# Optimization experiments

Measured on AMD Instinct MI355X. Metric: run time of the kernel, lower is better.

The kernel has to match this reference:

```python
import jax, jax.numpy as jnp
import numpy as np

NUM_HEADS = 16


def setup_inputs() -> dict:
    key = jax.random.key(0)
    ks = jax.random.split(key, 9)
    B, S, C = 2, 2048, 1024
    s = 1.0 / np.sqrt(C)
    return {
        "hidden_states": jax.random.normal(ks[0], (B, S, C), jnp.float32),
        "Wq": jax.random.normal(ks[1], (C, C), jnp.float32) * s,
        "bq": jnp.zeros((C,), jnp.float32),
        "Wk": jax.random.normal(ks[2], (C, C), jnp.float32) * s,
        "bk": jnp.zeros((C,), jnp.float32),
        "Wv": jax.random.normal(ks[3], (C, C), jnp.float32) * s,
        "bv": jnp.zeros((C,), jnp.float32),
        "Wo": jax.random.normal(ks[4], (C, C), jnp.float32) * s,
        "bo": jnp.zeros((C,), jnp.float32),
    }


def reference(hidden_states, Wq, bq, Wk, bk, Wv, bv, Wo, bo):
    # Self-attention path of AttnProcessor (3D input, no mask, no norms,
    # residual_connection=True, rescale_output_factor=1.0).
    B, S, C = hidden_states.shape
    H = NUM_HEADS
    D = C // H
    residual = hidden_states

    q = hidden_states @ Wq + bq  # [B,S,C]
    k = hidden_states @ Wk + bk
    v = hidden_states @ Wv + bv

    # head_to_batch_dim: [B,S,C] -> [B,S,H,D]
    q = q.reshape(B, S, H, D)
    k = k.reshape(B, S, H, D)
    v = v.reshape(B, S, H, D)

    scale = 1.0 / np.sqrt(D).astype(np.float32)
    # get_attention_scores: baddbmm with scale, then softmax (full [B,H,S,S])
    scores = jnp.einsum("bqhd,bkhd->bhqk", q, k) * scale
    probs = jax.nn.softmax(scores, axis=-1)

    out = jnp.einsum("bhqk,bkhd->bqhd", probs, v)  # bmm(probs, value)
    out = out.reshape(B, S, C)  # batch_to_head_dim

    out = out @ Wo + bo  # to_out[0]; to_out[1] is dropout (identity in eval)
    out = out + residual  # residual_connection
    return out  # rescale_output_factor = 1.0
```

## Files before the change

### kernel.cpp

```cpp
#include <hip/hip_runtime.h>

#define BATCH 2
#define SEQ   2048
#define CH    1024
#define NHEAD 16
#define HDIM  64
#define MROWS (BATCH * SEQ)

typedef __attribute__((ext_vector_type(8))) short short8;
typedef __attribute__((ext_vector_type(4))) float floatx4;
typedef unsigned short ushort_t;

__device__ __forceinline__ float b2f(ushort_t u) {
    union { unsigned int i; float f; } x;
    x.i = ((unsigned int)u) << 16;
    return x.f;
}
__device__ __forceinline__ ushort_t f2b(float f) {
    union { float f; unsigned int i; } x;
    x.f = f;
    unsigned int lsb = (x.i >> 16) & 1u;
    x.i += 0x7fffu + lsb;
    return (ushort_t)(x.i >> 16);
}
__device__ __forceinline__ unsigned pack2(float a, float b) {
    return (unsigned)f2b(a) | ((unsigned)f2b(b) << 16);
}
__device__ __forceinline__ unsigned cvt_pk_bf16(float a, float b) {
    unsigned r;
    asm("v_cvt_pk_bf16_f32 %0, %1, %2" : "=v"(r) : "v"(a), "v"(b));
    return r;
}

__device__ __forceinline__ void gld16(const ushort_t* g, ushort_t* l) {
    __builtin_amdgcn_global_load_lds(
        (const __attribute__((address_space(1))) void*)g,
        (__attribute__((address_space(3))) void*)l, 16, 0, 0);
}

template <int VM>
__device__ __forceinline__ void vm_barrier() {
    asm volatile("s_waitcnt vmcnt(%0) lgkmcnt(0)\n\ts_barrier" ::"i"(VM)
                 : "memory");
}

__global__ __launch_bounds__(256) void cvt_bf16_kernel(
    const float* __restrict__ in, ushort_t* __restrict__ out, int n4) {
    int i = blockIdx.x * blockDim.x + threadIdx.x;
    if (i < n4) {
        float4 v = ((const float4*)in)[i];
        ushort4 o = {f2b(v.x), f2b(v.y), f2b(v.z), f2b(v.w)};
        ((ushort4*)out)[i] = o;
    }
}

__global__ __launch_bounds__(256) void transpose_cvt_all(
    const float* __restrict__ W0, const float* __restrict__ W1,
    const float* __restrict__ W2, const float* __restrict__ W3,
    ushort_t* __restrict__ T0, ushort_t* __restrict__ T1,
    ushort_t* __restrict__ T2, ushort_t* __restrict__ T3) {
    __shared__ ushort_t T[64][68];
    const int z = blockIdx.z;
    const float* W = (z == 0) ? W0 : (z == 1) ? W1 : (z == 2) ? W2 : W3;
    ushort_t* Wt = (z == 0) ? T0 : (z == 1) ? T1 : (z == 2) ? T2 : T3;
    const int tid = threadIdx.x;
    const int n0 = blockIdx.x * 64, k0 = blockIdx.y * 64;
    const int r = tid >> 4, c4 = (tid & 15) * 4;
#pragma unroll
    for (int p = 0; p < 4; p++) {
        int k = p * 16 + r;
        float4 v = *(const float4*)&W[(size_t)(k0 + k) * CH + n0 + c4];
        T[c4 + 0][k] = f2b(v.x);
        T[c4 + 1][k] = f2b(v.y);
        T[c4 + 2][k] = f2b(v.z);
        T[c4 + 3][k] = f2b(v.w);
    }
    __syncthreads();
#pragma unroll
    for (int p = 0; p < 4; p++) {
        int n = p * 16 + r;
        ushort4 o = {T[n][c4 + 0], T[n][c4 + 1], T[n][c4 + 2], T[n][c4 + 3]};
        *(ushort4*)&Wt[(size_t)(n0 + n) * CH + k0 + c4] = o;
    }
}

__device__ __forceinline__ void gemm_core_db(
    const ushort_t* __restrict__ A, const ushort_t* __restrict__ Bt,
    int bm, int n0, int tid, floatx4 acc[4][4], ushort_t* lds) {
    const int wave = tid >> 6, lane = tid & 63;
    const int quad = lane >> 4, t16 = lane & 15;
    const int wm = wave >> 1, wn = wave & 1;
    const int arow = tid >> 2, ak = (tid & 3) * 8;

    const ushort_t* a0 = A + (size_t)(bm + arow) * CH + ak;
    const ushort_t* a1 = A + (size_t)(bm + 64 + arow) * CH + ak;
    const ushort_t* b0 = Bt + (size_t)(n0 + arow) * CH + ak;
    const ushort_t* b1 = Bt + (size_t)(n0 + 64 + arow) * CH + ak;

#pragma unroll
    for (int i = 0; i < 4; i++)
#pragma unroll
        for (int j = 0; j < 4; j++) acc[i][j] = (floatx4){0.f, 0.f, 0.f, 0.f};

    auto stage = [&](int k, ushort_t* buf) {
        gld16(a0 + k, buf + wave * 512);
        gld16(a1 + k, buf + 2048 + wave * 512);
        gld16(b0 + k, buf + 4096 + wave * 512);
        gld16(b1 + k, buf + 6144 + wave * 512);
    };
    auto compute = [&](const ushort_t* As) {
        const ushort_t* Bs = As + 4096;
        short8 af[4], bf[4];
#pragma unroll
        for (int i = 0; i < 4; i++)
            af[i] = *(const short8*)&As[(wm * 64 + i * 16 + t16) * 32 + quad * 8];
#pragma unroll
        for (int j = 0; j < 4; j++)
            bf[j] = *(const short8*)&Bs[(wn * 64 + j * 16 + t16) * 32 + quad * 8];
#pragma unroll
        for (int i = 0; i < 4; i++)
#pragma unroll
            for (int j = 0; j < 4; j++)
                acc[i][j] = __builtin_amdgcn_mfma_f32_16x16x32_bf16(
                    af[i], bf[j], acc[i][j], 0, 0, 0);
    };

    ushort_t* bcur = lds;
    ushort_t* bnext = lds + 8192;
    ushort_t* bfar = lds + 16384;

    stage(0, bcur);
    stage(32, bnext);

    for (int it = 0; it < CH / 32 - 2; ++it) {
        vm_barrier<4>();
        stage((it + 2) * 32, bfar);
        compute(bcur);
        ushort_t* t = bcur; bcur = bnext; bnext = bfar; bfar = t;
    }
    vm_barrier<4>();
    compute(bcur);
    vm_barrier<0>();
    compute(bnext);
}

__global__ __launch_bounds__(256) void gemm_qkv(
    const ushort_t* __restrict__ X,
    const ushort_t* __restrict__ WqT, const ushort_t* __restrict__ WkT,
    const ushort_t* __restrict__ WvT,
    const float* __restrict__ bq, const float* __restrict__ bk,
    const float* __restrict__ bv,
    ushort_t* __restrict__ Qm, ushort_t* __restrict__ Km,
    ushort_t* __restrict__ Vtm) {
    __shared__ ushort_t lds[3 * 8192];
    const int tid = threadIdx.x;
    const int seg = blockIdx.x >> 3;
    const int n0 = (blockIdx.x & 7) * 128;
    const int bm = blockIdx.y * 128;
    const ushort_t* Bt = (seg == 0) ? WqT : (seg == 1) ? WkT : WvT;
    const float* bias = (seg == 0) ? bq : (seg == 1) ? bk : bv;

    floatx4 acc[4][4];
    gemm_core_db(X, Bt, bm, n0, tid, acc, lds);

    const int lane = tid & 63, wave = tid >> 6;
    const int quad = lane >> 4, t16 = lane & 15;
    const int wm = wave >> 1, wn = wave & 1;

    if (seg < 2) {
        ushort_t* outp = seg ? Km : Qm;
        const float sc = seg ? 1.0f : 0.125f;
#pragma unroll
        for (int i = 0; i < 4; i++)
#pragma unroll
            for (int j = 0; j < 4; j++) {
                const int col = n0 + wn * 64 + j * 16 + t16;
                const float bb = bias[col];
                const int row0 = bm + wm * 64 + i * 16 + quad * 4;
#pragma unroll
                for (int r = 0; r < 4; r++)
                    outp[(size_t)(row0 + r) * CH + col] =
                        f2b((acc[i][j][r] + bb) * sc);
            }
    } else {
        ushort_t* rep = lds;
        const int b = bm >> 11;
        const int s_base = bm & (SEQ - 1);
#pragma unroll
        for (int half = 0; half < 2; half++) {
            __syncthreads();
            if (wn == half) {
#pragma unroll
                for (int i = 0; i < 4; i++)
#pragma unroll
                    for (int j = 0; j < 4; j++) {
                        const int dl = j * 16 + t16;
                        const int sl = wm * 64 + i * 16 + quad * 4;
                        const float bb = bias[n0 + half * 64 + dl];
                        uint2 w = {pack2(acc[i][j][0] + bb, acc[i][j][1] + bb),
                                   pack2(acc[i][j][2] + bb, acc[i][j][3] + bb)};
                        *(uint2*)&rep[dl * 136 + sl] = w;
                    }
            }
            __syncthreads();
#pragma unroll
            for (int step = 0; step < 4; step++) {
                const int dl = step * 16 + (tid >> 4);
                const int sl = (tid & 15) * 8;
                short8 v = *(const short8*)&rep[dl * 136 + sl];
                const int col = n0 + half * 64 + dl;
                const int h = col >> 6, dd = col & 63;
                const int c = (sl >> 3) & 7;
                const int r7 = dd & 7;
                const int slot0 = (c & 4) | ((2 * c) & 3);
                const int slot1 = (c & 4) | ((2 * c + 1) & 3);
                const int sub = ((c >> 1) & 1) << 2;
                ushort_t* vrow = Vtm +
                    (((size_t)b * NHEAD + h) * HDIM + dd) * SEQ + s_base +
                    (sl & 64);
                union { short8 s; uint2 u[2]; } vv;
                vv.s = v;
                *(uint2*)&vrow[((slot0 ^ r7) << 3) + sub] = vv.u[0];
                *(uint2*)&vrow[((slot1 ^ r7) << 3) + sub] = vv.u[1];
            }
        }
    }
}

__global__ __launch_bounds__(256) void gemm_out(
    const ushort_t* __restrict__ Am, const ushort_t* __restrict__ WoT,
    const float* __restrict__ bo, const float* __restrict__ resid,
    float* __restrict__ out) {
    __shared__ ushort_t lds[3 * 6144];
    const int tid = threadIdx.x;
    const int n0 = blockIdx.x * 64;
    const int bm = blockIdx.y * 128;
    const int wave = tid >> 6, lane = tid & 63;
    const int quad = lane >> 4, t16 = lane & 15;
    const int arow = tid >> 2, ak = (tid & 3) * 8;

    const ushort_t* a0 = Am + (size_t)(bm + arow) * CH + ak;
    const ushort_t* a1 = Am + (size_t)(bm + 64 + arow) * CH + ak;
    const ushort_t* b0 = WoT + (size_t)(n0 + arow) * CH + ak;

    floatx4 acc[2][4];
#pragma unroll
    for (int i = 0; i < 2; i++)
#pragma unroll
        for (int j = 0; j < 4; j++) acc[i][j] = (floatx4){0.f, 0.f, 0.f, 0.f};

    auto stage = [&](int k, ushort_t* buf) {
        gld16(a0 + k, buf + wave * 512);
        gld16(a1 + k, buf + 2048 + wave * 512);
        gld16(b0 + k, buf + 4096 + wave * 512);
    };
    auto compute = [&](const ushort_t* As) {
        const ushort_t* Bs = As + 4096;
        short8 af[2], bf[4];
#pragma unroll
        for (int i = 0; i < 2; i++)
            af[i] = *(const short8*)&As[(wave * 32 + i * 16 + t16) * 32 + quad * 8];
#pragma unroll
        for (int j = 0; j < 4; j++)
            bf[j] = *(const short8*)&Bs[(j * 16 + t16) * 32 + quad * 8];
#pragma unroll
        for (int i = 0; i < 2; i++)
#pragma unroll
            for (int j = 0; j < 4; j++)
                acc[i][j] = __builtin_amdgcn_mfma_f32_16x16x32_bf16(
                    af[i], bf[j], acc[i][j], 0, 0, 0);
    };

    ushort_t* bcur = lds;
    ushort_t* bnext = lds + 6144;
    ushort_t* bfar = lds + 12288;

    stage(0, bcur);
    stage(32, bnext);

    for (int it = 0; it < CH / 32 - 2; ++it) {
        vm_barrier<3>();
        stage((it + 2) * 32, bfar);
        compute(bcur);
        ushort_t* t = bcur; bcur = bnext; bnext = bfar; bfar = t;
    }
    vm_barrier<3>();
    compute(bcur);
    vm_barrier<0>();
    compute(bnext);

#pragma unroll
    for (int i = 0; i < 2; i++)
#pragma unroll
        for (int j = 0; j < 4; j++) {
            const int col = n0 + j * 16 + t16;
            const float bb = bo[col];
            const int row0 = bm + wave * 32 + i * 16 + quad * 4;
#pragma unroll
            for (int r = 0; r < 4; r++) {
                const size_t idx = (size_t)(row0 + r) * CH + col;
                out[idx] = acc[i][j][r] + bb + resid[idx];
            }
        }
}

__global__ __launch_bounds__(512, 4) void flash_attn_mfma(
    const ushort_t* __restrict__ Q, const ushort_t* __restrict__ K,
    const ushort_t* __restrict__ Vt, ushort_t* __restrict__ O) {
    __shared__ __attribute__((aligned(16))) ushort_t smem[2][2][64][64];

    const int tid = threadIdx.x;
    const int wave = tid >> 6, lane = tid & 63;
    const int quad = lane >> 4, t16 = lane & 15;
    const int bh = blockIdx.y, b = bh >> 4, h = bh & 15;
    const int q0 = blockIdx.x * 128;

    const size_t base_q = ((size_t)b * SEQ) * CH + (size_t)h * HDIM;
    const size_t base_vt = ((size_t)(b * NHEAD + h)) * HDIM * SEQ;

    short8 qf[2];
    {
        const ushort_t* qp =
            Q + base_q + (size_t)(q0 + wave * 16 + t16) * CH + quad * 8;
        qf[0] = *(const short8*)(qp);
        qf[1] = *(const short8*)(qp + 32);
    }

    const short8 ones = (short8)(short)0x3F80;

    floatx4 Oa[4];
    floatx4 Oe = (floatx4){0.f, 0.f, 0.f, 0.f};
#pragma unroll
    for (int d = 0; d < 4; d++) Oa[d] = (floatx4){0.f, 0.f, 0.f, 0.f};

    const int sr = tid >> 3;
    const int ss = tid & 7;
    const ushort_t* ksrc = K + base_q + (size_t)sr * CH + ((ss ^ (sr & 7)) << 3);
    const ushort_t* vsrc = Vt + base_vt + (size_t)sr * SEQ + (ss << 3);

    auto stage = [&](int k0, int buf) {
        gld16(ksrc + (size_t)k0 * CH, &smem[buf][0][0][0] + wave * 512);
        gld16(vsrc + k0, &smem[buf][1][0][0] + wave * 512);
    };

    const int koff0 = (quad ^ (t16 & 7)) << 3;
    const int koff1 = ((quad + 4) ^ (t16 & 7)) << 3;

    stage(0, 0);

    for (int t = 0; t < SEQ / 64; ++t) {
        vm_barrier<0>();
        if (t + 1 < SEQ / 64) stage((t + 1) * 64, (t + 1) & 1);
        const ushort_t* Kb = &smem[t & 1][0][0][0];
        const ushort_t* Vb = &smem[t & 1][1][0][0];

        uint2 pw[4];
#pragma unroll
        for (int j = 0; j < 4; j++) {
            short8 kf0 = *(const short8*)&Kb[(j * 16 + t16) * 64 + koff0];
            short8 kf1 = *(const short8*)&Kb[(j * 16 + t16) * 64 + koff1];
            floatx4 z = (floatx4){0.f, 0.f, 0.f, 0.f};
            z = __builtin_amdgcn_mfma_f32_16x16x32_bf16(kf0, qf[0], z, 0, 0, 0);
            z = __builtin_amdgcn_mfma_f32_16x16x32_bf16(kf1, qf[1], z, 0, 0, 0);
            pw[j].x = cvt_pk_bf16(__expf(z[0]), __expf(z[1]));
            pw[j].y = cvt_pk_bf16(__expf(z[2]), __expf(z[3]));
        }
        short8 pf0, pf1;
        {
            union { uint4 u; short8 s; } c0, c1;
            c0.u = (uint4){pw[0].x, pw[0].y, pw[1].x, pw[1].y};
            c1.u = (uint4){pw[2].x, pw[2].y, pw[3].x, pw[3].y};
            pf0 = c0.s;
            pf1 = c1.s;
        }

        __builtin_amdgcn_s_setprio(1);
#pragma unroll
        for (int d = 0; d < 4; d++) {
            short8 vf0 = *(const short8*)&Vb[(d * 16 + t16) * 64 + koff0];
            short8 vf1 = *(const short8*)&Vb[(d * 16 + t16) * 64 + koff1];
            Oa[d] = __builtin_amdgcn_mfma_f32_16x16x32_bf16(pf0, vf0, Oa[d], 0, 0, 0);
            Oa[d] = __builtin_amdgcn_mfma_f32_16x16x32_bf16(pf1, vf1, Oa[d], 0, 0, 0);
        }
        Oe = __builtin_amdgcn_mfma_f32_16x16x32_bf16(pf0, ones, Oe, 0, 0, 0);
        Oe = __builtin_amdgcn_mfma_f32_16x16x32_bf16(pf1, ones, Oe, 0, 0, 0);
        __builtin_amdgcn_s_setprio(0);
    }

    float inv[4];
#pragma unroll
    for (int r = 0; r < 4; r++) inv[r] = 1.f / Oe[r];
#pragma unroll
    for (int d = 0; d < 4; d++)
#pragma unroll
        for (int r = 0; r < 4; r++) {
            const int row = q0 + wave * 16 + quad * 4 + r;
            O[base_q + (size_t)row * CH + d * 16 + t16] =
                f2b(Oa[d][r] * inv[r]);
        }
}

extern "C" void kernel_launch(void* const* d_in, const int* in_sizes, int n_in,
                              void* d_out, int out_size, void* d_ws,
                              size_t ws_size, hipStream_t stream) {
    const float* X  = (const float*)d_in[0];
    const float* Wq = (const float*)d_in[1];
    const float* bq = (const float*)d_in[2];
    const float* Wk = (const float*)d_in[3];
    const float* bk = (const float*)d_in[4];
    const float* Wv = (const float*)d_in[5];
    const float* bv = (const float*)d_in[6];
    const float* Wo = (const float*)d_in[7];
    const float* bo = (const float*)d_in[8];
    float* out = (float*)d_out;

    const size_t MC = (size_t)MROWS * CH;
    const size_t WC = (size_t)CH * CH;
    ushort_t* ws  = (ushort_t*)d_ws;
    ushort_t* X16 = ws;
    ushort_t* Am  = ws;
    ushort_t* Qm  = ws + MC;
    ushort_t* Km  = ws + 2 * MC;
    ushort_t* Vtm = ws + 3 * MC;
    ushort_t* WqT = ws + 4 * MC;
    ushort_t* WkT = ws + 4 * MC + WC;
    ushort_t* WvT = ws + 4 * MC + 2 * WC;
    ushort_t* WoT = ws + 4 * MC + 3 * WC;

    dim3 blk(256);

    cvt_bf16_kernel<<<dim3((MC / 4 + 255) / 256), blk, 0, stream>>>(X, X16, (int)(MC / 4));
    transpose_cvt_all<<<dim3(16, 16, 4), blk, 0, stream>>>(
        Wq, Wk, Wv, Wo, WqT, WkT, WvT, WoT);

    gemm_qkv<<<dim3(24, 32), blk, 0, stream>>>(X16, WqT, WkT, WvT, bq, bk, bv,
                                               Qm, Km, Vtm);

    flash_attn_mfma<<<dim3(SEQ / 128, BATCH * NHEAD), dim3(512), 0, stream>>>(
        Qm, Km, Vtm, Am);

    gemm_out<<<dim3(16, 32), blk, 0, stream>>>(Am, WoT, bo, X, out);
}
```

Measured before the change: 189.1 us.

## Process two 16-row query tiles per wave in flash attention to reuse K/V fragments

Each wave now handles 32 query rows instead of 16, so every K and V fragment read from shared memory feeds two sets of MFMAs. The block covers 256 queries, which halves both the grid and the global K/V staging traffic per query. In exchange it doubles accumulator and P-fragment registers and relaxes launch bounds to 2 blocks per CU. That lowers occupancy, and 256 blocks may underfill the GPU.

Measured after the change: 186.5 us. No clear change (-1.4%).

```diff
diff --git a/kernel.cpp b/kernel.cpp
--- a/kernel.cpp
+++ b/kernel.cpp
@@ -304,7 +304,7 @@
         }
 }
 
-__global__ __launch_bounds__(512, 4) void flash_attn_mfma(
+__global__ __launch_bounds__(512, 2) void flash_attn_mfma(
     const ushort_t* __restrict__ Q, const ushort_t* __restrict__ K,
     const ushort_t* __restrict__ Vt, ushort_t* __restrict__ O) {
     __shared__ __attribute__((aligned(16))) ushort_t smem[2][2][64][64];
@@ -313,25 +313,30 @@
     const int wave = tid >> 6, lane = tid & 63;
     const int quad = lane >> 4, t16 = lane & 15;
     const int bh = blockIdx.y, b = bh >> 4, h = bh & 15;
-    const int q0 = blockIdx.x * 128;
+    const int q0 = blockIdx.x * 256;
 
     const size_t base_q = ((size_t)b * SEQ) * CH + (size_t)h * HDIM;
     const size_t base_vt = ((size_t)(b * NHEAD + h)) * HDIM * SEQ;
 
-    short8 qf[2];
-    {
+    short8 qf[2][2];
+#pragma unroll
+    for (int u = 0; u < 2; u++) {
         const ushort_t* qp =
-            Q + base_q + (size_t)(q0 + wave * 16 + t16) * CH + quad * 8;
-        qf[0] = *(const short8*)(qp);
-        qf[1] = *(const short8*)(qp + 32);
+            Q + base_q + (size_t)(q0 + wave * 32 + u * 16 + t16) * CH + quad * 8;
+        qf[u][0] = *(const short8*)(qp);
+        qf[u][1] = *(const short8*)(qp + 32);
     }
 
     const short8 ones = (short8)(short)0x3F80;
 
-    floatx4 Oa[4];
-    floatx4 Oe = (floatx4){0.f, 0.f, 0.f, 0.f};
-#pragma unroll
-    for (int d = 0; d < 4; d++) Oa[d] = (floatx4){0.f, 0.f, 0.f, 0.f};
+    floatx4 Oa[2][4];
+    floatx4 Oe[2];
+#pragma unroll
+    for (int u = 0; u < 2; u++) {
+        Oe[u] = (floatx4){0.f, 0.f, 0.f, 0.f};
+#pragma unroll
+        for (int d = 0; d < 4; d++) Oa[u][d] = (floatx4){0.f, 0.f, 0.f, 0.f};
+    }
 
     const int sr = tid >> 3;
     const int ss = tid & 7;
@@ -354,24 +359,28 @@
         const ushort_t* Kb = &smem[t & 1][0][0][0];
         const ushort_t* Vb = &smem[t & 1][1][0][0];
 
-        uint2 pw[4];
+        uint2 pw[2][4];
 #pragma unroll
         for (int j = 0; j < 4; j++) {
             short8 kf0 = *(const short8*)&Kb[(j * 16 + t16) * 64 + koff0];
             short8 kf1 = *(const short8*)&Kb[(j * 16 + t16) * 64 + koff1];
-            floatx4 z = (floatx4){0.f, 0.f, 0.f, 0.f};
-            z = __builtin_amdgcn_mfma_f32_16x16x32_bf16(kf0, qf[0], z, 0, 0, 0);
-            z = __builtin_amdgcn_mfma_f32_16x16x32_bf16(kf1, qf[1], z, 0, 0, 0);
-            pw[j].x = cvt_pk_bf16(__expf(z[0]), __expf(z[1]));
-            pw[j].y = cvt_pk_bf16(__expf(z[2]), __expf(z[3]));
-        }
-        short8 pf0, pf1;
-        {
-            union { uint4 u; short8 s; } c0, c1;
-            c0.u = (uint4){pw[0].x, pw[0].y, pw[1].x, pw[1].y};
-            c1.u = (uint4){pw[2].x, pw[2].y, pw[3].x, pw[3].y};
-            pf0 = c0.s;
-            pf1 = c1.s;
+#pragma unroll
+            for (int u = 0; u < 2; u++) {
+                floatx4 z = (floatx4){0.f, 0.f, 0.f, 0.f};
+                z = __builtin_amdgcn_mfma_f32_16x16x32_bf16(kf0, qf[u][0], z, 0, 0, 0);
+                z = __builtin_amdgcn_mfma_f32_16x16x32_bf16(kf1, qf[u][1], z, 0, 0, 0);
+                pw[u][j].x = cvt_pk_bf16(__expf(z[0]), __expf(z[1]));
+                pw[u][j].y = cvt_pk_bf16(__expf(z[2]), __expf(z[3]));
+            }
+        }
+        short8 pf[2][2];
+#pragma unroll
+        for (int u = 0; u < 2; u++) {
+            union { uint4 q; short8 s; } cc;
+            cc.q = (uint4){pw[u][0].x, pw[u][0].y, pw[u][1].x, pw[u][1].y};
+            pf[u][0] = cc.s;
+            cc.q = (uint4){pw[u][2].x, pw[u][2].y, pw[u][3].x, pw[u][3].y};
+            pf[u][1] = cc.s;
         }
 
         __builtin_amdgcn_s_setprio(1);
@@ -379,25 +388,34 @@
         for (int d = 0; d < 4; d++) {
             short8 vf0 = *(const short8*)&Vb[(d * 16 + t16) * 64 + koff0];
             short8 vf1 = *(const short8*)&Vb[(d * 16 + t16) * 64 + koff1];
-            Oa[d] = __builtin_amdgcn_mfma_f32_16x16x32_bf16(pf0, vf0, Oa[d], 0, 0, 0);
-            Oa[d] = __builtin_amdgcn_mfma_f32_16x16x32_bf16(pf1, vf1, Oa[d], 0, 0, 0);
-        }
-        Oe = __builtin_amdgcn_mfma_f32_16x16x32_bf16(pf0, ones, Oe, 0, 0, 0);
-        Oe = __builtin_amdgcn_mfma_f32_16x16x32_bf16(pf1, ones, Oe, 0, 0, 0);
+#pragma unroll
+            for (int u = 0; u < 2; u++) {
+                Oa[u][d] = __builtin_amdgcn_mfma_f32_16x16x32_bf16(pf[u][0], vf0, Oa[u][d], 0, 0, 0);
+                Oa[u][d] = __builtin_amdgcn_mfma_f32_16x16x32_bf16(pf[u][1], vf1, Oa[u][d], 0, 0, 0);
+            }
+        }
+#pragma unroll
+        for (int u = 0; u < 2; u++) {
+            Oe[u] = __builtin_amdgcn_mfma_f32_16x16x32_bf16(pf[u][0], ones, Oe[u], 0, 0, 0);
+            Oe[u] = __builtin_amdgcn_mfma_f32_16x16x32_bf16(pf[u][1], ones, Oe[u], 0, 0, 0);
+        }
         __builtin_amdgcn_s_setprio(0);
     }
 
-    float inv[4];
-#pragma unroll
-    for (int r = 0; r < 4; r++) inv[r] = 1.f / Oe[r];
-#pragma unroll
-    for (int d = 0; d < 4; d++)
-#pragma unroll
-        for (int r = 0; r < 4; r++) {
-            const int row = q0 + wave * 16 + quad * 4 + r;
-            O[base_q + (size_t)row * CH + d * 16 + t16] =
-                f2b(Oa[d][r] * inv[r]);
-        }
+#pragma unroll
+    for (int u = 0; u < 2; u++) {
+        float inv[4];
+#pragma unroll
+        for (int r = 0; r < 4; r++) inv[r] = 1.f / Oe[u][r];
+#pragma unroll
+        for (int d = 0; d < 4; d++)
+#pragma unroll
+            for (int r = 0; r < 4; r++) {
+                const int row = q0 + wave * 32 + u * 16 + quad * 4 + r;
+                O[base_q + (size_t)row * CH + d * 16 + t16] =
+                    f2b(Oa[u][d][r] * inv[r]);
+            }
+    }
 }
 
 extern "C" void kernel_launch(void* const* d_in, const int* in_sizes, int n_in,
@@ -436,7 +454,7 @@
     gemm_qkv<<<dim3(24, 32), blk, 0, stream>>>(X16, WqT, WkT, WvT, bq, bk, bv,
                                                Qm, Km, Vtm);
 
-    flash_attn_mfma<<<dim3(SEQ / 128, BATCH * NHEAD), dim3(512), 0, stream>>>(
+    flash_attn_mfma<<<dim3(SEQ / 256, BATCH * NHEAD), dim3(512), 0, stream>>>(
         Qm, Km, Vtm, Am);
 
     gemm_out<<<dim3(16, 32), blk, 0, stream>>>(Am, WoT, bo, X, out);
```
